# Performance work log

Measured on AMD Instinct MI355X. Metric: run time of the kernel, lower is better.

## Reference

```python
import jax, jax.numpy as jnp
import numpy as np

B, D, H1, H2, E, O = 32768, 256, 512, 256, 16, 64


def setup_inputs() -> dict:
    key = jax.random.key(0)
    ks = jax.random.split(key, 12)
    s = lambda fan_in: 1.0 / np.sqrt(fan_in)
    return {
        "x": jax.random.normal(ks[0], (B, D), dtype=jnp.float32),
        "gate_w": jax.random.normal(ks[1], (D, E), dtype=jnp.float32) * s(D),
        "gate_b": jnp.zeros((E,), dtype=jnp.float32),
        "W1": jax.random.normal(ks[2], (E, D, H1), dtype=jnp.float32) * s(D),
        "b1": jnp.zeros((E, H1), dtype=jnp.float32),
        "W2": jax.random.normal(ks[3], (E, H1, H2), dtype=jnp.float32) * s(H1),
        "b2": jnp.zeros((E, H2), dtype=jnp.float32),
        "W3": jax.random.normal(ks[4], (E, H2, O), dtype=jnp.float32) * s(H2),
        "b3": jnp.zeros((E, O), dtype=jnp.float32),
        "head_w": jax.random.normal(ks[5], (O, 1), dtype=jnp.float32) * s(O),
        "head_b": jnp.zeros((1,), dtype=jnp.float32),
    }


def reference(x, gate_w, gate_b, W1, b1, W2, b2, W3, b3, head_w, head_b):
    # gating: softmax over experts, [B, E]
    gates = jax.nn.softmax(x @ gate_w + gate_b, axis=-1)
    # all-expert dense MLP as batched GEMMs over leading expert axis
    h1 = jax.nn.relu(jnp.einsum('bd,edh->ebh', x, W1) + b1[:, None, :])   # [E,B,H1]
    h2 = jax.nn.relu(jnp.einsum('ebh,ehk->ebk', h1, W2) + b2[:, None, :])  # [E,B,H2]
    eo = jnp.einsum('ebk,eko->ebo', h2, W3) + b3[:, None, :]               # [E,B,O]
    # gated combination: sum_e gates[b,e] * eo[e,b,:]
    fused = jnp.einsum('be,ebo->bo', gates, eo)                            # [B,O]
    yts = (fused @ head_w + head_b)[:, 0]                                  # [B]
    return yts
```

## Files before the change

### kernel.cpp

```cpp
#include <hip/hip_runtime.h>

#define B_TOK 32768
#define D_IN  256
#define H1D   512
#define H2D   256
#define NE    16
#define NO    64
#define TK    128

typedef _Float16 half8 __attribute__((ext_vector_type(8)));
typedef _Float16 half4 __attribute__((ext_vector_type(4)));
typedef float   float4_t __attribute__((ext_vector_type(4)));

__global__ void prep_kernel(const float* __restrict__ W1, const float* __restrict__ W2,
                            const float* __restrict__ W3, const float* __restrict__ b3,
                            const float* __restrict__ hw, const float* __restrict__ gw,
                            _Float16* __restrict__ w1p, _Float16* __restrict__ w2p,
                            float* __restrict__ w3h, float* __restrict__ c3,
                            _Float16* __restrict__ gwp) {
  int blk = blockIdx.x;
  int tid = threadIdx.x;
  if (blk < 1024) {
    int t = blk * 256 + tid;
    int lane = t & 63;
    int kt   = (t >> 6) & 7;
    int ntg  = (t >> 9) & 31;
    int e    = t >> 14;
    int n  = ntg * 16 + (lane & 15);
    int kb = kt * 32 + (lane >> 4) * 8;
    half8 v;
    #pragma unroll
    for (int j = 0; j < 8; ++j)
      v[j] = (_Float16)W1[((size_t)(e * D_IN + kb + j)) * H1D + n];
    *(half8*)(w1p + (size_t)t * 8) = v;
  } else if (blk < 2048) {
    int t = (blk - 1024) * 256 + tid;
    int lane = t & 63;
    int ktg  = (t >> 6) & 15;
    int ntg  = (t >> 10) & 15;
    int e    = t >> 14;
    int n  = ntg * 16 + (lane & 15);
    int kb = ktg * 32 + (lane >> 4) * 8;
    half8 v;
    #pragma unroll
    for (int j = 0; j < 8; ++j)
      v[j] = (_Float16)W2[((size_t)(e * H1D + kb + j)) * H2D + n];
    *(half8*)(w2p + (size_t)t * 8) = v;
  } else if (blk < 2065) {
    int t = (blk - 2048) * 256 + tid;
    if (t < NE * H2D) {
      int e = t >> 8, h = t & 255;
      float s = 0.f;
      #pragma unroll
      for (int o = 0; o < NO; ++o) s = fmaf(W3[((size_t)(e * H2D + h)) * NO + o], hw[o], s);
      w3h[t] = s;
    } else if (t < NE * H2D + NE) {
      int e = t - NE * H2D;
      float s = 0.f;
      #pragma unroll
      for (int o = 0; o < NO; ++o) s = fmaf(b3[e * NO + o], hw[o], s);
      c3[e] = s;
    }
  } else {
    for (int t = tid; t < 512; t += 256) {
      int lane = t & 63;
      int kt   = t >> 6;
      int e  = lane & 15;
      int kb = kt * 32 + (lane >> 4) * 8;
      half8 v;
      #pragma unroll
      for (int j = 0; j < 8; ++j)
        v[j] = (_Float16)gw[(kb + j) * NE + e];
      *(half8*)(gwp + (size_t)t * 8) = v;
    }
  }
}

__global__ __launch_bounds__(512, 2) void moe_main(
    const float* __restrict__ x,
    const float* __restrict__ b1,
    const float* __restrict__ b2,
    const _Float16* __restrict__ w1p,
    const _Float16* __restrict__ w2p,
    const _Float16* __restrict__ gwp,
    const float* __restrict__ gb,
    const float* __restrict__ w3h,
    const float* __restrict__ c3,
    const float* __restrict__ head_b,
    float* __restrict__ out) {
  __shared__ _Float16 x_lds[64 * 512];
  __shared__ _Float16 h1c[64 * 512];
  __shared__ float g_lds[TK * 17];
  __shared__ float fin[8 * TK];

  const int tid  = threadIdx.x;
  const int w    = tid >> 6;
  const int lane = tid & 63;
  const int q    = lane >> 4;
  const int l16  = lane & 15;
  const int m0   = blockIdx.x * TK;

  #pragma unroll
  for (int f = 0; f < 8; ++f) {
    const float* xr = x + (size_t)(m0 + w * 16 + l16) * D_IN + f * 32 + q * 8;
    float4_t v0 = *(const float4_t*)(xr);
    float4_t v1 = *(const float4_t*)(xr + 4);
    half8 h;
    h[0] = (_Float16)v0[0]; h[1] = (_Float16)v0[1];
    h[2] = (_Float16)v0[2]; h[3] = (_Float16)v0[3];
    h[4] = (_Float16)v1[0]; h[5] = (_Float16)v1[1];
    h[6] = (_Float16)v1[2]; h[7] = (_Float16)v1[3];
    *(half8*)(x_lds + (size_t)(w * 8 + f) * 512 + lane * 8) = h;
  }
  __syncthreads();

  {
    float gbv = gb[l16];
    float4_t lg = (float4_t){0.f, 0.f, 0.f, 0.f};
    #pragma unroll
    for (int kt = 0; kt < 8; ++kt) {
      half8 xa = *(const half8*)(x_lds + (size_t)(w * 8 + kt) * 512 + lane * 8);
      half8 bfr = *(const half8*)(gwp + (size_t)kt * 512 + lane * 8);
      lg = __builtin_amdgcn_mfma_f32_16x16x32_f16(xa, bfr, lg, 0, 0, 0);
    }
    #pragma unroll
    for (int r = 0; r < 4; ++r) {
      float v = lg[r] + gbv;
      float m = v;
      m = fmaxf(m, __shfl_xor(m, 1));
      m = fmaxf(m, __shfl_xor(m, 2));
      m = fmaxf(m, __shfl_xor(m, 4));
      m = fmaxf(m, __shfl_xor(m, 8));
      float p = __expf(v - m);
      float s = p;
      s += __shfl_xor(s, 1);
      s += __shfl_xor(s, 2);
      s += __shfl_xor(s, 4);
      s += __shfl_xor(s, 8);
      g_lds[(w * 16 + q * 4 + r) * 17 + l16] = p / s;
    }
  }

  float yacc[8][4];
  #pragma unroll
  for (int mt = 0; mt < 8; ++mt)
    #pragma unroll
    for (int r = 0; r < 4; ++r) yacc[mt][r] = 0.f;

  for (int e = 0; e < NE; ++e) {
    float4_t h2[8][2];
    #pragma unroll
    for (int mt = 0; mt < 8; ++mt)
      #pragma unroll
      for (int j = 0; j < 2; ++j)
        h2[mt][j] = (float4_t){0.f, 0.f, 0.f, 0.f};

    #pragma unroll
    for (int ch = 0; ch < 2; ++ch) {
      float4_t a1[2][8];
      #pragma unroll
      for (int i = 0; i < 2; ++i)
        #pragma unroll
        for (int nt = 0; nt < 8; ++nt)
          a1[i][nt] = (float4_t){0.f, 0.f, 0.f, 0.f};

      const _Float16* w1e =
          w1p + ((size_t)((e * 32 + ch * 16 + w * 2) * 8)) * 512 + lane * 8;
      #pragma unroll
      for (int kt = 0; kt < 8; ++kt) {
        half8 wc[2];
        #pragma unroll
        for (int i = 0; i < 2; ++i)
          wc[i] = *(const half8*)(w1e + (size_t)(i * 8 + kt) * 512);
        half8 xb[8];
        #pragma unroll
        for (int nt = 0; nt < 8; ++nt)
          xb[nt] = *(const half8*)(x_lds + (size_t)(nt * 8 + kt) * 512 + lane * 8);
        #pragma unroll
        for (int i = 0; i < 2; ++i)
          #pragma unroll
          for (int nt = 0; nt < 8; ++nt)
            a1[i][nt] = __builtin_amdgcn_mfma_f32_16x16x32_f16(
                wc[i], xb[nt], a1[i][nt], 0, 0, 0);
      }

      #pragma unroll
      for (int i = 0; i < 2; ++i) {
        int colbase = ch * 256 + (w * 2 + i) * 16 + q * 4;
        float4_t bb = *(const float4_t*)(b1 + e * H1D + colbase);
        int qp = (i << 1) + (q >> 1);
        int fo = (qp * 16 + l16) * 8 + ((q & 1) << 2);
        #pragma unroll
        for (int nt = 0; nt < 8; ++nt) {
          half4 hv;
          #pragma unroll
          for (int r = 0; r < 4; ++r)
            hv[r] = (_Float16)fmaxf(a1[i][nt][r] + bb[r], 0.f);
          *(half4*)(h1c + (size_t)(nt * 8 + w) * 512 + fo) = hv;
        }
      }

      __syncthreads();

      const _Float16* w2e =
          w2p + ((size_t)((e * 16 + w * 2) * 16 + ch * 8)) * 512 + lane * 8;
      #pragma unroll
      for (int kt = 0; kt < 8; ++kt) {
        half8 w2c[2];
        #pragma unroll
        for (int j = 0; j < 2; ++j)
          w2c[j] = *(const half8*)(w2e + (size_t)(j * 16 + kt) * 512);
        half8 hac[8];
        #pragma unroll
        for (int mt = 0; mt < 8; ++mt)
          hac[mt] = *(const half8*)(h1c + (size_t)(mt * 8 + kt) * 512 + lane * 8);
        #pragma unroll
        for (int mt = 0; mt < 8; ++mt)
          #pragma unroll
          for (int j = 0; j < 2; ++j)
            h2[mt][j] = __builtin_amdgcn_mfma_f32_16x16x32_f16(
                hac[mt], w2c[j], h2[mt][j], 0, 0, 0);
      }

      __syncthreads();
    }

    float b2v[2], w3v[2];
    #pragma unroll
    for (int j = 0; j < 2; ++j) {
      int n = (w * 2 + j) * 16 + l16;
      b2v[j] = b2[e * H2D + n];
      w3v[j] = w3h[e * H2D + n];
    }
    #pragma unroll
    for (int mt = 0; mt < 8; ++mt) {
      #pragma unroll
      for (int r = 0; r < 4; ++r) {
        float s = 0.f;
        #pragma unroll
        for (int j = 0; j < 2; ++j)
          s += fmaxf(h2[mt][j][r] + b2v[j], 0.f) * w3v[j];
        yacc[mt][r] += g_lds[(mt * 16 + q * 4 + r) * 17 + e] * s;
      }
    }
  }

  #pragma unroll
  for (int mt = 0; mt < 8; ++mt) {
    #pragma unroll
    for (int r = 0; r < 4; ++r) {
      float v = yacc[mt][r];
      v += __shfl_xor(v, 1);
      v += __shfl_xor(v, 2);
      v += __shfl_xor(v, 4);
      v += __shfl_xor(v, 8);
      yacc[mt][r] = v;
    }
  }
  if (l16 == 0) {
    #pragma unroll
    for (int mt = 0; mt < 8; ++mt)
      #pragma unroll
      for (int r = 0; r < 4; ++r)
        fin[w * TK + mt * 16 + q * 4 + r] = yacc[mt][r];
  }
  __syncthreads();
  if (tid < TK) {
    float sum = 0.f;
    #pragma unroll
    for (int k = 0; k < 8; ++k) sum += fin[k * TK + tid];
    float gc = 0.f;
    #pragma unroll
    for (int e = 0; e < NE; ++e) gc += g_lds[tid * 17 + e] * c3[e];
    out[m0 + tid] = sum + gc + head_b[0];
  }
}

extern "C" void kernel_launch(void* const* d_in, const int* in_sizes, int n_in,
                              void* d_out, int out_size, void* d_ws, size_t ws_size,
                              hipStream_t stream) {
  const float* x      = (const float*)d_in[0];
  const float* gate_w = (const float*)d_in[1];
  const float* gate_b = (const float*)d_in[2];
  const float* W1     = (const float*)d_in[3];
  const float* b1     = (const float*)d_in[4];
  const float* W2     = (const float*)d_in[5];
  const float* b2     = (const float*)d_in[6];
  const float* W3     = (const float*)d_in[7];
  const float* b3     = (const float*)d_in[8];
  const float* head_w = (const float*)d_in[9];
  const float* head_b = (const float*)d_in[10];
  float* out = (float*)d_out;

  char* ws = (char*)d_ws;
  _Float16* w1p = (_Float16*)(ws);
  _Float16* w2p = (_Float16*)(ws + 4194304);
  _Float16* gwp = (_Float16*)(ws + 8388608);
  float*    w3h = (float*)(ws + 8396800);
  float*    c3  = (float*)(ws + 8413184);

  hipLaunchKernelGGL(prep_kernel, dim3(2066), dim3(256), 0, stream,
                     W1, W2, W3, b3, head_w, gate_w, w1p, w2p, w3h, c3, gwp);
  hipLaunchKernelGGL(moe_main, dim3(B_TOK / TK), dim3(512), 0, stream,
                     x, b1, b2, w1p, w2p, gwp, gate_b, w3h, c3, head_b, out);
}
```

Baseline: 359.1 us.

## Transpose weights through LDS in prep, prefetch W2 fragments, raise MFMA priority

The prep kernel now loads W1/W2 rows with coalesced float4 reads, converts them to fp16 into a padded LDS tile, and then writes the MFMA-packed layout from LDS. This replaces the strided per-element global gathers and cuts the grid from 2066 to 402 blocks. The main kernel issues the first half of each chunk's W2 fragment loads before the barrier, so they overlap the h1 store and sync. It also wraps the MFMA loops in s_setprio to favour matrix issue. The prefetch adds 8 half8 registers per thread, which could lower occupancy.

Measured after the change: 338.7 us. 1.06x faster.

```diff
diff --git a/kernel.cpp b/kernel.cpp
--- a/kernel.cpp
+++ b/kernel.cpp
@@ -18,36 +18,61 @@
                             _Float16* __restrict__ w1p, _Float16* __restrict__ w2p,
                             float* __restrict__ w3h, float* __restrict__ c3,
                             _Float16* __restrict__ gwp) {
-  int blk = blockIdx.x;
-  int tid = threadIdx.x;
-  if (blk < 1024) {
-    int t = blk * 256 + tid;
-    int lane = t & 63;
-    int kt   = (t >> 6) & 7;
-    int ntg  = (t >> 9) & 31;
-    int e    = t >> 14;
-    int n  = ntg * 16 + (lane & 15);
-    int kb = kt * 32 + (lane >> 4) * 8;
-    half8 v;
-    #pragma unroll
-    for (int j = 0; j < 8; ++j)
-      v[j] = (_Float16)W1[((size_t)(e * D_IN + kb + j)) * H1D + n];
-    *(half8*)(w1p + (size_t)t * 8) = v;
-  } else if (blk < 2048) {
-    int t = (blk - 1024) * 256 + tid;
-    int lane = t & 63;
-    int ktg  = (t >> 6) & 15;
-    int ntg  = (t >> 10) & 15;
-    int e    = t >> 14;
-    int n  = ntg * 16 + (lane & 15);
-    int kb = ktg * 32 + (lane >> 4) * 8;
-    half8 v;
-    #pragma unroll
-    for (int j = 0; j < 8; ++j)
-      v[j] = (_Float16)W2[((size_t)(e * H1D + kb + j)) * H2D + n];
-    *(half8*)(w2p + (size_t)t * 8) = v;
-  } else if (blk < 2065) {
-    int t = (blk - 2048) * 256 + tid;
+  __shared__ _Float16 tile[32 * 516];
+  const int blk = blockIdx.x;
+  const int tid = threadIdx.x;
+
+  if (blk < 128) {
+    const int e = blk >> 3, kt = blk & 7;
+    const float* src = W1 + ((size_t)(e * D_IN + kt * 32)) * H1D;
+    #pragma unroll
+    for (int it = 0; it < 16; ++it) {
+      int idx = it * 256 + tid;
+      int r = idx >> 7, c4 = idx & 127;
+      float4_t v = *(const float4_t*)(src + (size_t)r * H1D + c4 * 4);
+      half4 h;
+      h[0] = (_Float16)v[0]; h[1] = (_Float16)v[1];
+      h[2] = (_Float16)v[2]; h[3] = (_Float16)v[3];
+      *(half4*)(tile + r * 516 + c4 * 4) = h;
+    }
+    __syncthreads();
+    const int lane = tid & 63, wv = tid >> 6;
+    #pragma unroll
+    for (int it = 0; it < 8; ++it) {
+      int ntg = it * 4 + wv;
+      half8 v;
+      #pragma unroll
+      for (int j = 0; j < 8; ++j)
+        v[j] = tile[((lane >> 4) * 8 + j) * 516 + ntg * 16 + (lane & 15)];
+      *(half8*)(w1p + ((size_t)(((e * 32 + ntg) * 8 + kt) * 64 + lane)) * 8) = v;
+    }
+  } else if (blk < 384) {
+    const int b2i = blk - 128;
+    const int e = b2i >> 4, ktg = b2i & 15;
+    const float* src = W2 + ((size_t)(e * H1D + ktg * 32)) * H2D;
+    #pragma unroll
+    for (int it = 0; it < 8; ++it) {
+      int idx = it * 256 + tid;
+      int r = idx >> 6, c4 = idx & 63;
+      float4_t v = *(const float4_t*)(src + (size_t)r * H2D + c4 * 4);
+      half4 h;
+      h[0] = (_Float16)v[0]; h[1] = (_Float16)v[1];
+      h[2] = (_Float16)v[2]; h[3] = (_Float16)v[3];
+      *(half4*)(tile + r * 260 + c4 * 4) = h;
+    }
+    __syncthreads();
+    const int lane = tid & 63, wv = tid >> 6;
+    #pragma unroll
+    for (int it = 0; it < 4; ++it) {
+      int ntg = it * 4 + wv;
+      half8 v;
+      #pragma unroll
+      for (int j = 0; j < 8; ++j)
+        v[j] = tile[((lane >> 4) * 8 + j) * 260 + ntg * 16 + (lane & 15)];
+      *(half8*)(w2p + ((size_t)(((e * 16 + ntg) * 16 + ktg) * 64 + lane)) * 8) = v;
+    }
+  } else if (blk < 401) {
+    int t = (blk - 384) * 256 + tid;
     if (t < NE * H2D) {
       int e = t >> 8, h = t & 255;
       float s = 0.f;
@@ -166,6 +191,7 @@
 
       const _Float16* w1e =
           w1p + ((size_t)((e * 32 + ch * 16 + w * 2) * 8)) * 512 + lane * 8;
+      __builtin_amdgcn_s_setprio(1);
       #pragma unroll
       for (int kt = 0; kt < 8; ++kt) {
         half8 wc[2];
@@ -183,6 +209,7 @@
             a1[i][nt] = __builtin_amdgcn_mfma_f32_16x16x32_f16(
                 wc[i], xb[nt], a1[i][nt], 0, 0, 0);
       }
+      __builtin_amdgcn_s_setprio(0);
 
       #pragma unroll
       for (int i = 0; i < 2; ++i) {
@@ -200,16 +227,25 @@
         }
       }
 
-      __syncthreads();
-
       const _Float16* w2e =
           w2p + ((size_t)((e * 16 + w * 2) * 16 + ch * 8)) * 512 + lane * 8;
+      half8 w2pre[2][4];
+      #pragma unroll
+      for (int j = 0; j < 2; ++j)
+        #pragma unroll
+        for (int kt = 0; kt < 4; ++kt)
+          w2pre[j][kt] = *(const half8*)(w2e + (size_t)(j * 16 + kt) * 512);
+
+      __syncthreads();
+
+      __builtin_amdgcn_s_setprio(1);
       #pragma unroll
       for (int kt = 0; kt < 8; ++kt) {
         half8 w2c[2];
         #pragma unroll
         for (int j = 0; j < 2; ++j)
-          w2c[j] = *(const half8*)(w2e + (size_t)(j * 16 + kt) * 512);
+          w2c[j] = (kt < 4) ? w2pre[j][kt]
+                            : *(const half8*)(w2e + (size_t)(j * 16 + kt) * 512);
         half8 hac[8];
         #pragma unroll
         for (int mt = 0; mt < 8; ++mt)
@@ -221,6 +257,7 @@
             h2[mt][j] = __builtin_amdgcn_mfma_f32_16x16x32_f16(
                 hac[mt], w2c[j], h2[mt][j], 0, 0, 0);
       }
+      __builtin_amdgcn_s_setprio(0);
 
       __syncthreads();
     }
@@ -299,7 +336,7 @@
   float*    w3h = (float*)(ws + 8396800);
   float*    c3  = (float*)(ws + 8413184);
 
-  hipLaunchKernelGGL(prep_kernel, dim3(2066), dim3(256), 0, stream,
+  hipLaunchKernelGGL(prep_kernel, dim3(402), dim3(256), 0, stream,
                      W1, W2, W3, b3, head_w, gate_w, w1p, w2p, w3h, c3, gwp);
   hipLaunchKernelGGL(moe_main, dim3(B_TOK / TK), dim3(512), 0, stream,
                      x, b1, b2, w1p, w2p, gwp, gate_b, w3h, c3, head_b, out);
```
